# Kernel tuning notes

Measured on AMD Instinct MI355X. Metric: run time of the kernel, lower is better.

Reference implementation:

```python
import jax, jax.numpy as jnp
import numpy as np

N_NODES = 100000

def _norm_coeffs(edge_index, n_nodes):
    # PyG GCNConv default: add self-loops, symmetric normalization D^-1/2 A D^-1/2
    src = jnp.concatenate([edge_index[0], jnp.arange(n_nodes, dtype=edge_index.dtype)])
    dst = jnp.concatenate([edge_index[1], jnp.arange(n_nodes, dtype=edge_index.dtype)])
    deg = jax.ops.segment_sum(jnp.ones_like(dst, dtype=jnp.float32), dst, num_segments=n_nodes)
    dinv = jnp.where(deg > 0, jax.lax.rsqrt(deg), 0.0)
    norm = dinv[src] * dinv[dst]  # [E + N]
    return src, dst, norm

def _gcn_conv(x, W, b, src, dst, norm, n_nodes):
    h = x @ W                       # [N, out] dense transform first (PyG order)
    msg = h[src] * norm[:, None]    # gather + scale, [E+N, out]
    out = jax.ops.segment_sum(msg, dst, num_segments=n_nodes)  # scatter-add aggregate
    return out + b

def setup_inputs() -> dict:
    key = jax.random.key(0)
    ks = jax.random.split(key, 8)
    in_feats, h_feats, num_classes = 128, 128, 64
    n_edges = 1_600_000
    x = jax.random.normal(ks[0], (N_NODES, in_feats), dtype=jnp.float32)
    edge_index = jax.random.randint(ks[1], (2, n_edges), 0, N_NODES, dtype=jnp.int64)
    def glorot(k, fi, fo):
        s = jnp.sqrt(6.0 / (fi + fo))
        return jax.random.uniform(k, (fi, fo), jnp.float32, -s, s)
    return {
        "x": x,
        "edge_index": edge_index,
        "W0": glorot(ks[2], in_feats, h_feats), "b0": jnp.zeros((h_feats,), jnp.float32),
        "W1": glorot(ks[3], h_feats, h_feats), "b1": jnp.zeros((h_feats,), jnp.float32),
        "W2": glorot(ks[4], h_feats, num_classes), "b2": jnp.zeros((num_classes,), jnp.float32),
    }

def reference(x, edge_index, W0, b0, W1, b1, W2, b2):
    n_nodes = x.shape[0]
    src, dst, norm = _norm_coeffs(edge_index, n_nodes)
    # layer 0 + 1: ReLU between (dropout is identity in eval mode)
    h = jax.nn.relu(_gcn_conv(x, W0, b0, src, dst, norm, n_nodes))
    h = jax.nn.relu(_gcn_conv(h, W1, b1, src, dst, norm, n_nodes))
    # final layer: no activation
    return _gcn_conv(h, W2, b2, src, dst, norm, n_nodes)
```

## Files before the change

kernel.cpp:

```cpp
#include <hip/hip_runtime.h>
#include <hip/hip_bf16.h>
#include <stdint.h>


typedef __attribute__((ext_vector_type(8))) short bf16x8;
typedef __attribute__((ext_vector_type(4))) float f32x4;

__device__ __forceinline__ float bflo(uint32_t u) { return __uint_as_float(u << 16); }
__device__ __forceinline__ float bfhi(uint32_t u) { return __uint_as_float(u & 0xffff0000u); }
__device__ __forceinline__ unsigned short f2bf(float f) {
    uint32_t x = __float_as_uint(f);
    return (unsigned short)((x + 0x7fffu + ((x >> 16) & 1u)) >> 16);
}

__device__ __forceinline__ int xcc_id() {
    int x;
    asm volatile("s_getreg_b32 %0, hwreg(HW_REG_XCC_ID)" : "=s"(x));
    return x & 7;
}

__global__ __launch_bounds__(256) void k_deg_rank(const int* __restrict__ dst,
                                                  int* __restrict__ scnt,
                                                  int* __restrict__ rank,
                                                  int N, int E) {
    int e = blockIdx.x * 256 + threadIdx.x;
    int xc = xcc_id();
    if (e < E) {
        int r = atomicAdd(&scnt[xc * N + dst[e]], 1);
        rank[e] = (xc << 28) | r;
    }
}

__global__ __launch_bounds__(256) void k_merge(int* __restrict__ scnt,
                                               int* __restrict__ deg,
                                               float* __restrict__ dinv,
                                               unsigned short* __restrict__ hzero,
                                               int N) {
    int i = blockIdx.x * 256 + threadIdx.x;
    if (blockIdx.x == 0 && threadIdx.x < 16) {
        uint4 z; z.x = 0; z.y = 0; z.z = 0; z.w = 0;
        ((uint4*)hzero)[threadIdx.x] = z;
    }
    if (i >= N) return;
    int sum = 0;
#pragma unroll
    for (int s = 0; s < 8; ++s) {
        int c = scnt[s * N + i];
        scnt[s * N + i] = sum;
        sum += c;
    }
    deg[i] = sum;
    dinv[i] = rsqrtf((float)(sum + 1));
}

__global__ __launch_bounds__(256) void k_scan_local(const int* __restrict__ deg,
                                                    int* __restrict__ incl,
                                                    int* __restrict__ bsum, int N) {
    __shared__ int part[256];
    int t = threadIdx.x;
    int idx0 = blockIdx.x * 1024 + t * 4;
    int4 lv = {0, 0, 0, 0};
    if (idx0 + 4 <= N) {
        lv = *(const int4*)&deg[idx0];
    } else {
        int* pv = (int*)&lv;
        for (int i = 0; i < 4; ++i) pv[i] = (idx0 + i < N) ? deg[idx0 + i] : 0;
    }
    int s = lv.x + lv.y + lv.z + lv.w;
    part[t] = s;
    __syncthreads();
    for (int off = 1; off < 256; off <<= 1) {
        int x = (t >= off) ? part[t - off] : 0;
        __syncthreads();
        part[t] += x;
        __syncthreads();
    }
    int run = (t == 0) ? 0 : part[t - 1];
    if (t == 255) bsum[blockIdx.x] = part[255];
    int4 ov;
    ov.x = run + lv.x;
    ov.y = ov.x + lv.y;
    ov.z = ov.y + lv.z;
    ov.w = ov.z + lv.w;
    if (idx0 + 4 <= N) {
        *(int4*)&incl[idx0] = ov;
    } else {
        int* po = (int*)&ov;
        for (int i = 0; i < 4; ++i)
            if (idx0 + i < N) incl[idx0 + i] = po[i];
    }
}

__global__ __launch_bounds__(256) void k_scan_tops(int* __restrict__ bsum, int nb,
                                                   int* __restrict__ row_ptr, int N) {
    __shared__ int part[256];
    int t = threadIdx.x;
    int v = (t < nb) ? bsum[t] : 0;
    part[t] = v;
    __syncthreads();
    for (int off = 1; off < 256; off <<= 1) {
        int x = (t >= off) ? part[t - off] : 0;
        __syncthreads();
        part[t] += x;
        __syncthreads();
    }
    if (t < nb) bsum[t] = part[t] - v;
    if (t == 255) row_ptr[N] = part[255];
}

__global__ __launch_bounds__(256) void k_scan_final(const int* __restrict__ incl,
                                                    const int* __restrict__ deg,
                                                    const int* __restrict__ bsum,
                                                    int* __restrict__ row_ptr, int N) {
    int i = blockIdx.x * 256 + threadIdx.x;
    if (i < N) row_ptr[i] = incl[i] - deg[i] + bsum[i >> 10];
}

__global__ __launch_bounds__(256) void k_scatter(const int* __restrict__ src,
                                                 const int* __restrict__ dst,
                                                 const int* __restrict__ rank,
                                                 const int* __restrict__ row_ptr,
                                                 const int* __restrict__ scnt,
                                                 int* __restrict__ col_idx,
                                                 int N, int E) {
    int e = blockIdx.x * 256 + threadIdx.x;
    if (e < E) {
        int d = dst[e];
        int pr = rank[e];
        int s = pr >> 28, lr = pr & 0x0fffffff;
        col_idx[row_ptr[d] + scnt[s * N + d] + lr] = src[e];
    }
}

__global__ __launch_bounds__(256) void k_prepw(const float* __restrict__ W0,
                                               const float* __restrict__ W1,
                                               const float* __restrict__ W2,
                                               unsigned short* __restrict__ wt0,
                                               unsigned short* __restrict__ wt1,
                                               unsigned short* __restrict__ wt2) {
    int id = blockIdx.x * 256 + threadIdx.x;
    const float* Wsrc;
    unsigned short* dst;
    int t, M, plane;
    if (id < 16384)      { t = id;         Wsrc = W0; dst = wt0; M = 128; plane = 16384; }
    else if (id < 32768) { t = id - 16384; Wsrc = W1; dst = wt1; M = 128; plane = 16384; }
    else if (id < 40960) { t = id - 32768; Wsrc = W2; dst = wt2; M = 64;  plane = 8192;  }
    else return;
    int k = (M == 128) ? (t >> 7) : (t >> 6);
    int c = (M == 128) ? (t & 127) : (t & 63);
    float v = Wsrc[k * M + c];
    unsigned short hi = f2bf(v);
    float lov = v - bflo((uint32_t)hi);
    dst[c * 128 + k]         = hi;
    dst[plane + c * 128 + k] = f2bf(lov);
}

template <int NCOL>
__global__ __launch_bounds__(256) void k_gemm_mfma(
    const float* __restrict__ A, const unsigned short* __restrict__ Wt,
    const float* __restrict__ dinv, unsigned short* __restrict__ H, int N) {
    constexpr int K = 128, KT = 64;
    constexpr int A_PLANE = 128 * KT;
    constexpr int W_PLANE = NCOL * KT;
    __shared__ __align__(16) unsigned short sm[2 * A_PLANE + 2 * W_PLANE];
    unsigned short* Ah  = sm;
    unsigned short* Al  = sm + A_PLANE;
    unsigned short* Whp = sm + 2 * A_PLANE;
    unsigned short* Wlp = sm + 2 * A_PLANE + W_PLANE;

    const int tid = threadIdx.x;
    const long r0 = (long)blockIdx.x * 128;
    const int w = tid >> 6, l = tid & 63;
    const int lr = l & 15, lk = l >> 4;
    constexpr int WR = (NCOL == 128) ? 4 : 2;
    const int wrow = (NCOL == 128) ? (w >> 1) * 64 : w * 32;
    const int wcol = (NCOL == 128) ? (w & 1) * 64 : 0;

    f32x4 acc[WR][4];
#pragma unroll
    for (int i = 0; i < WR; ++i)
#pragma unroll
        for (int j = 0; j < 4; ++j) acc[i][j] = (f32x4){0.f, 0.f, 0.f, 0.f};

    for (int kt = 0; kt < 2; ++kt) {
        if (kt) __syncthreads();
#pragma unroll
        for (int it = 0; it < 4; ++it) {
            int id = it * 256 + tid;
            int r = id >> 3, kc = id & 7;
            long gr = r0 + r;
            if (gr >= N) gr = N - 1;
            const float* ap = &A[gr * K + kt * KT + kc * 8];
            float4 v0 = *(const float4*)ap;
            float4 v1 = *(const float4*)(ap + 4);
            float vv[8] = {v0.x, v0.y, v0.z, v0.w, v1.x, v1.y, v1.z, v1.w};
            union { unsigned short u[8]; bf16x8 v; } ph, pl;
#pragma unroll
            for (int j = 0; j < 8; ++j) {
                unsigned short h = f2bf(vv[j]);
                ph.u[j] = h;
                pl.u[j] = f2bf(vv[j] - bflo((uint32_t)h));
            }
            int boff = r * 128 + ((kc * 16) ^ ((r & 7) << 4));
            *(bf16x8*)((char*)Ah + boff) = ph.v;
            *(bf16x8*)((char*)Al + boff) = pl.v;
        }
#pragma unroll
        for (int it = 0; it < NCOL / 32; ++it) {
            int id = it * 256 + tid;
            int c = id >> 3, kc = id & 7;
            const unsigned short* wp = &Wt[c * K + kt * KT + kc * 8];
            bf16x8 vh = *(const bf16x8*)wp;
            bf16x8 vl = *(const bf16x8*)(wp + NCOL * K);
            int boff = c * 128 + ((kc * 16) ^ ((c & 7) << 4));
            *(bf16x8*)((char*)Whp + boff) = vh;
            *(bf16x8*)((char*)Wlp + boff) = vl;
        }
        __syncthreads();
#pragma unroll
        for (int ks = 0; ks < 2; ++ks) {
            int kb = ks * 64 + lk * 16;
            bf16x8 bh[4], bl[4];
#pragma unroll
            for (int cf = 0; cf < 4; ++cf) {
                int c = wcol + cf * 16 + lr;
                int off = c * 128 + (kb ^ ((c & 7) << 4));
                bh[cf] = *(bf16x8*)((char*)Whp + off);
                bl[cf] = *(bf16x8*)((char*)Wlp + off);
            }
#pragma unroll
            for (int rf = 0; rf < WR; ++rf) {
                int r = wrow + rf * 16 + lr;
                int off = r * 128 + (kb ^ ((r & 7) << 4));
                bf16x8 ah = *(bf16x8*)((char*)Ah + off);
                bf16x8 al = *(bf16x8*)((char*)Al + off);
#pragma unroll
                for (int cf = 0; cf < 4; ++cf) {
                    acc[rf][cf] = __builtin_amdgcn_mfma_f32_16x16x32_bf16(ah, bh[cf], acc[rf][cf], 0, 0, 0);
                    acc[rf][cf] = __builtin_amdgcn_mfma_f32_16x16x32_bf16(al, bh[cf], acc[rf][cf], 0, 0, 0);
                    acc[rf][cf] = __builtin_amdgcn_mfma_f32_16x16x32_bf16(ah, bl[cf], acc[rf][cf], 0, 0, 0);
                }
            }
        }
    }
#pragma unroll
    for (int rf = 0; rf < WR; ++rf) {
        long rb = r0 + wrow + rf * 16 + lk * 4;
#pragma unroll
        for (int reg = 0; reg < 4; ++reg) {
            long r = rb + reg;
            if (r < N) {
                float dv = dinv[r];
#pragma unroll
                for (int cf = 0; cf < 4; ++cf) {
                    int c = wcol + cf * 16 + lr;
                    H[r * NCOL + c] = f2bf(dv * acc[rf][cf][reg]);
                }
            }
        }
    }
}

template <int F, bool RELU>
__global__ __launch_bounds__(256) void k_agg(const unsigned short* __restrict__ H,
                                             const int* __restrict__ row_ptr,
                                             const int* __restrict__ col_idx,
                                             const float* __restrict__ dinv,
                                             const float* __restrict__ bias,
                                             float* __restrict__ Y, int N) {
    constexpr int FL = F / 32;
    int lane = threadIdx.x & 63;
    int node = blockIdx.x * 4 + (threadIdx.x >> 6);
    if (node >= N) return;
    const int half = lane >> 5, hl = lane & 31;
    const int DUMMY = (F == 128) ? N : 2 * N;

    float acc[FL];
    if constexpr (F == 128) {
        if (half == 0) {
            uint64_t u = *(const uint64_t*)&H[(size_t)node * 128 + hl * 4];
            acc[0] = bflo((uint32_t)u);         acc[1] = bfhi((uint32_t)u);
            acc[2] = bflo((uint32_t)(u >> 32)); acc[3] = bfhi((uint32_t)(u >> 32));
        } else { acc[0] = acc[1] = acc[2] = acc[3] = 0.f; }
    } else {
        if (half == 0) {
            uint32_t u = *(const uint32_t*)&H[(size_t)node * 64 + hl * 2];
            acc[0] = bflo(u); acc[1] = bfhi(u);
        } else { acc[0] = acc[1] = 0.f; }
    }

    int start = row_ptr[node], end = row_ptr[node + 1];
    for (int base = start; base < end; base += 64) {
        int idx = DUMMY;
        if (base + lane < end) idx = col_idx[base + lane];
        int cnt = min(64, end - base);
        for (int j = 0; j < cnt; j += 8) {
            int s0 = __shfl(idx, j + half);
            int s1 = __shfl(idx, j + 2 + half);
            int s2 = __shfl(idx, j + 4 + half);
            int s3 = __shfl(idx, j + 6 + half);
            if constexpr (F == 128) {
                uint64_t u0 = *(const uint64_t*)&H[(size_t)s0 * 128 + hl * 4];
                uint64_t u1 = *(const uint64_t*)&H[(size_t)s1 * 128 + hl * 4];
                uint64_t u2 = *(const uint64_t*)&H[(size_t)s2 * 128 + hl * 4];
                uint64_t u3 = *(const uint64_t*)&H[(size_t)s3 * 128 + hl * 4];
                acc[0] += bflo((uint32_t)u0);         acc[1] += bfhi((uint32_t)u0);
                acc[2] += bflo((uint32_t)(u0 >> 32)); acc[3] += bfhi((uint32_t)(u0 >> 32));
                acc[0] += bflo((uint32_t)u1);         acc[1] += bfhi((uint32_t)u1);
                acc[2] += bflo((uint32_t)(u1 >> 32)); acc[3] += bfhi((uint32_t)(u1 >> 32));
                acc[0] += bflo((uint32_t)u2);         acc[1] += bfhi((uint32_t)u2);
                acc[2] += bflo((uint32_t)(u2 >> 32)); acc[3] += bfhi((uint32_t)(u2 >> 32));
                acc[0] += bflo((uint32_t)u3);         acc[1] += bfhi((uint32_t)u3);
                acc[2] += bflo((uint32_t)(u3 >> 32)); acc[3] += bfhi((uint32_t)(u3 >> 32));
            } else {
                uint32_t u0 = *(const uint32_t*)&H[(size_t)s0 * 64 + hl * 2];
                uint32_t u1 = *(const uint32_t*)&H[(size_t)s1 * 64 + hl * 2];
                uint32_t u2 = *(const uint32_t*)&H[(size_t)s2 * 64 + hl * 2];
                uint32_t u3 = *(const uint32_t*)&H[(size_t)s3 * 64 + hl * 2];
                acc[0] += bflo(u0); acc[1] += bfhi(u0);
                acc[0] += bflo(u1); acc[1] += bfhi(u1);
                acc[0] += bflo(u2); acc[1] += bfhi(u2);
                acc[0] += bflo(u3); acc[1] += bfhi(u3);
            }
        }
    }

    float part[FL];
#pragma unroll
    for (int f = 0; f < FL; ++f) part[f] = __shfl_xor(acc[f], 32);
    if (half == 0) {
        float dv = dinv[node];
        if constexpr (F == 128) {
            float4 b = *(const float4*)&bias[hl * 4];
            float4 o;
            o.x = dv * (acc[0] + part[0]) + b.x;
            o.y = dv * (acc[1] + part[1]) + b.y;
            o.z = dv * (acc[2] + part[2]) + b.z;
            o.w = dv * (acc[3] + part[3]) + b.w;
            if (RELU) {
                o.x = fmaxf(o.x, 0.f); o.y = fmaxf(o.y, 0.f);
                o.z = fmaxf(o.z, 0.f); o.w = fmaxf(o.w, 0.f);
            }
            *(float4*)&Y[(size_t)node * 128 + hl * 4] = o;
        } else {
            float2 b = *(const float2*)&bias[hl * 2];
            float2 o;
            o.x = dv * (acc[0] + part[0]) + b.x;
            o.y = dv * (acc[1] + part[1]) + b.y;
            if (RELU) { o.x = fmaxf(o.x, 0.f); o.y = fmaxf(o.y, 0.f); }
            *(float2*)&Y[(size_t)node * 64 + hl * 2] = o;
        }
    }
}

extern "C" void kernel_launch(void* const* d_in, const int* in_sizes, int n_in,
                              void* d_out, int out_size, void* d_ws, size_t ws_size,
                              hipStream_t stream) {
    const float* x  = (const float*)d_in[0];
    const int* eidx = (const int*)d_in[1];
    const float* W0 = (const float*)d_in[2];
    const float* b0 = (const float*)d_in[3];
    const float* W1 = (const float*)d_in[4];
    const float* b1 = (const float*)d_in[5];
    const float* W2 = (const float*)d_in[6];
    const float* b2 = (const float*)d_in[7];
    float* out = (float*)d_out;

    const int N = in_sizes[0] / 128;
    const int E = in_sizes[1] / 2;
    const int* srcp = eidx;
    const int* dstp = eidx + E;

    char* p = (char*)d_ws;
    auto take = [&](size_t bytes) {
        char* r = p;
        p += (bytes + 255) & ~(size_t)255;
        return r;
    };
    int*            scnt    = (int*)take((size_t)8 * N * 4);
    int*            deg     = (int*)take((size_t)N * 4);
    int*            rank    = (int*)take((size_t)E * 4);
    int*            row_ptr = (int*)take((size_t)(N + 1) * 4);
    float*          dinv    = (float*)take((size_t)N * 4);
    int*            col_idx = (int*)take((size_t)E * 4);
    unsigned short* hbuf    = (unsigned short*)take((size_t)(N + 1) * 128 * 2);
    float*          ybuf    = (float*)take((size_t)N * 128 * 4);
    int*            incl    = (int*)take((size_t)N * 4);
    int*            bsum    = (int*)take((size_t)256 * 4);
    unsigned short* wt0     = (unsigned short*)take((size_t)2 * 16384 * 2);
    unsigned short* wt1     = (unsigned short*)take((size_t)2 * 16384 * 2);
    unsigned short* wt2     = (unsigned short*)take((size_t)2 * 8192 * 2);

    hipMemsetAsync(scnt, 0, (size_t)8 * N * 4, stream);

    k_deg_rank<<<(E + 255) / 256, 256, 0, stream>>>(dstp, scnt, rank, N, E);
    k_merge<<<(N + 255) / 256, 256, 0, stream>>>(scnt, deg, dinv,
                                                 hbuf + (size_t)N * 128, N);
    k_prepw<<<160, 256, 0, stream>>>(W0, W1, W2, wt0, wt1, wt2);

    int nb = (N + 1023) / 1024;
    k_scan_local<<<nb, 256, 0, stream>>>(deg, incl, bsum, N);
    k_scan_tops<<<1, 256, 0, stream>>>(bsum, nb, row_ptr, N);
    k_scan_final<<<(N + 255) / 256, 256, 0, stream>>>(incl, deg, bsum, row_ptr, N);

    k_scatter<<<(E + 255) / 256, 256, 0, stream>>>(srcp, dstp, rank, row_ptr,
                                                   scnt, col_idx, N, E);

    int gemm_grid = (N + 127) / 128;
    int agg_grid  = (N + 3) / 4;

    k_gemm_mfma<128><<<gemm_grid, 256, 0, stream>>>(x, wt0, dinv, hbuf, N);
    k_agg<128, true><<<agg_grid, 256, 0, stream>>>(hbuf, row_ptr, col_idx,
                                                   dinv, b0, ybuf, N);
    k_gemm_mfma<128><<<gemm_grid, 256, 0, stream>>>(ybuf, wt1, dinv, hbuf, N);
    k_agg<128, true><<<agg_grid, 256, 0, stream>>>(hbuf, row_ptr, col_idx,
                                                   dinv, b1, ybuf, N);
    k_gemm_mfma<64><<<gemm_grid, 256, 0, stream>>>(ybuf, wt2, dinv, hbuf, N);
    k_agg<64, false><<<agg_grid, 256, 0, stream>>>(hbuf, row_ptr, col_idx,
                                                   dinv, b2, out, N);
}
```

Measured before the change: 437.4 us.

## Partition CSR build by node range per XCD instead of per-XCC counters

Degree counting and scatter now launch 8 blocks per edge chunk. Each block handles only destinations in its eighth of the node range, so atomics on a given node come from one XCD under round-robin dispatch. The per-XCC count array, the rank array and the merge kernel are removed, and dinv computation and the zero row move into the scan finalize kernel. In exchange, each edge chunk's dst is read eight times, and the scatter order within a row becomes nondeterministic.

```diff
diff --git a/kernel.cpp b/kernel.cpp
--- a/kernel.cpp
+++ b/kernel.cpp
@@ -13,44 +13,22 @@
     return (unsigned short)((x + 0x7fffu + ((x >> 16) & 1u)) >> 16);
 }
 
-__device__ __forceinline__ int xcc_id() {
-    int x;
-    asm volatile("s_getreg_b32 %0, hwreg(HW_REG_XCC_ID)" : "=s"(x));
-    return x & 7;
-}
-
-__global__ __launch_bounds__(256) void k_deg_rank(const int* __restrict__ dst,
-                                                  int* __restrict__ scnt,
-                                                  int* __restrict__ rank,
-                                                  int N, int E) {
-    int e = blockIdx.x * 256 + threadIdx.x;
-    int xc = xcc_id();
-    if (e < E) {
-        int r = atomicAdd(&scnt[xc * N + dst[e]], 1);
-        rank[e] = (xc << 28) | r;
-    }
-}
-
-__global__ __launch_bounds__(256) void k_merge(int* __restrict__ scnt,
-                                               int* __restrict__ deg,
-                                               float* __restrict__ dinv,
-                                               unsigned short* __restrict__ hzero,
-                                               int N) {
-    int i = blockIdx.x * 256 + threadIdx.x;
-    if (blockIdx.x == 0 && threadIdx.x < 16) {
-        uint4 z; z.x = 0; z.y = 0; z.z = 0; z.w = 0;
-        ((uint4*)hzero)[threadIdx.x] = z;
-    }
-    if (i >= N) return;
-    int sum = 0;
-#pragma unroll
-    for (int s = 0; s < 8; ++s) {
-        int c = scnt[s * N + i];
-        scnt[s * N + i] = sum;
-        sum += c;
-    }
-    deg[i] = sum;
-    dinv[i] = rsqrtf((float)(sum + 1));
+#define EDGES_PER_CHUNK 4096
+
+__global__ __launch_bounds__(256) void k_deg(const int* __restrict__ dst,
+                                             int* __restrict__ deg,
+                                             int NS, int E) {
+    int v = blockIdx.x & 7;
+    int base = (blockIdx.x >> 3) * EDGES_PER_CHUNK;
+    int lo = v * NS, hi = lo + NS;
+#pragma unroll
+    for (int i = 0; i < EDGES_PER_CHUNK / 256; ++i) {
+        int e = base + i * 256 + threadIdx.x;
+        if (e < E) {
+            int d = dst[e];
+            if (d >= lo && d < hi) atomicAdd(&deg[d], 1);
+        }
+    }
 }
 
 __global__ __launch_bounds__(256) void k_scan_local(const int* __restrict__ deg,
@@ -111,24 +89,41 @@
 __global__ __launch_bounds__(256) void k_scan_final(const int* __restrict__ incl,
                                                     const int* __restrict__ deg,
                                                     const int* __restrict__ bsum,
-                                                    int* __restrict__ row_ptr, int N) {
+                                                    int* __restrict__ row_ptr,
+                                                    float* __restrict__ dinv,
+                                                    unsigned short* __restrict__ hzero,
+                                                    int N) {
     int i = blockIdx.x * 256 + threadIdx.x;
-    if (i < N) row_ptr[i] = incl[i] - deg[i] + bsum[i >> 10];
+    if (blockIdx.x == 0 && threadIdx.x < 16) {
+        uint4 z; z.x = 0; z.y = 0; z.z = 0; z.w = 0;
+        ((uint4*)hzero)[threadIdx.x] = z;
+    }
+    if (i < N) {
+        int dg = deg[i];
+        row_ptr[i] = incl[i] - dg + bsum[i >> 10];
+        dinv[i] = rsqrtf((float)(dg + 1));
+    }
 }
 
 __global__ __launch_bounds__(256) void k_scatter(const int* __restrict__ src,
                                                  const int* __restrict__ dst,
-                                                 const int* __restrict__ rank,
                                                  const int* __restrict__ row_ptr,
-                                                 const int* __restrict__ scnt,
+                                                 int* __restrict__ cursor,
                                                  int* __restrict__ col_idx,
-                                                 int N, int E) {
-    int e = blockIdx.x * 256 + threadIdx.x;
-    if (e < E) {
-        int d = dst[e];
-        int pr = rank[e];
-        int s = pr >> 28, lr = pr & 0x0fffffff;
-        col_idx[row_ptr[d] + scnt[s * N + d] + lr] = src[e];
+                                                 int NS, int E) {
+    int v = blockIdx.x & 7;
+    int base = (blockIdx.x >> 3) * EDGES_PER_CHUNK;
+    int lo = v * NS, hi = lo + NS;
+#pragma unroll
+    for (int i = 0; i < EDGES_PER_CHUNK / 256; ++i) {
+        int e = base + i * 256 + threadIdx.x;
+        if (e < E) {
+            int d = dst[e];
+            if (d >= lo && d < hi) {
+                int pos = row_ptr[d] + atomicAdd(&cursor[d], 1);
+                col_idx[pos] = src[e];
+            }
+        }
     }
 }
 
@@ -377,9 +372,8 @@
         p += (bytes + 255) & ~(size_t)255;
         return r;
     };
-    int*            scnt    = (int*)take((size_t)8 * N * 4);
     int*            deg     = (int*)take((size_t)N * 4);
-    int*            rank    = (int*)take((size_t)E * 4);
+    int*            cursor  = (int*)take((size_t)N * 4);
     int*            row_ptr = (int*)take((size_t)(N + 1) * 4);
     float*          dinv    = (float*)take((size_t)N * 4);
     int*            col_idx = (int*)take((size_t)E * 4);
@@ -391,20 +385,23 @@
     unsigned short* wt1     = (unsigned short*)take((size_t)2 * 16384 * 2);
     unsigned short* wt2     = (unsigned short*)take((size_t)2 * 8192 * 2);
 
-    hipMemsetAsync(scnt, 0, (size_t)8 * N * 4, stream);
-
-    k_deg_rank<<<(E + 255) / 256, 256, 0, stream>>>(dstp, scnt, rank, N, E);
-    k_merge<<<(N + 255) / 256, 256, 0, stream>>>(scnt, deg, dinv,
-                                                 hbuf + (size_t)N * 128, N);
+    hipMemsetAsync(deg, 0, (size_t)N * 4, stream);
+    hipMemsetAsync(cursor, 0, (size_t)N * 4, stream);
+
+    const int NS = (N + 7) / 8;
+    const int nch = (E + EDGES_PER_CHUNK - 1) / EDGES_PER_CHUNK;
+
+    k_deg<<<8 * nch, 256, 0, stream>>>(dstp, deg, NS, E);
     k_prepw<<<160, 256, 0, stream>>>(W0, W1, W2, wt0, wt1, wt2);
 
     int nb = (N + 1023) / 1024;
     k_scan_local<<<nb, 256, 0, stream>>>(deg, incl, bsum, N);
     k_scan_tops<<<1, 256, 0, stream>>>(bsum, nb, row_ptr, N);
-    k_scan_final<<<(N + 255) / 256, 256, 0, stream>>>(incl, deg, bsum, row_ptr, N);
-
-    k_scatter<<<(E + 255) / 256, 256, 0, stream>>>(srcp, dstp, rank, row_ptr,
-                                                   scnt, col_idx, N, E);
+    k_scan_final<<<(N + 255) / 256, 256, 0, stream>>>(incl, deg, bsum, row_ptr,
+                                                      dinv, hbuf + (size_t)N * 128, N);
+
+    k_scatter<<<8 * nch, 256, 0, stream>>>(srcp, dstp, row_ptr, cursor,
+                                           col_idx, NS, E);
 
     int gemm_grid = (N + 127) / 128;
     int agg_grid  = (N + 3) / 4;
```

New measurement: 484.7 us. 1.11x slower.
